# Performance work log

Measured on AMD Instinct MI355X. Metric: run time of the kernel, lower is better.

The kernel has to match this reference:

```python
import jax, jax.numpy as jnp
import numpy as np

NUM_CLASSES = 4
IMG_SIZE = 640.0
NUM_ANCHORS = 3
EPS = 1e-07


def _giou(px, py, pw, ph, tx, ty, tw, th):
    # corners
    x1n, y1n, x1x, y1x = px - pw / 2, py - ph / 2, px + pw / 2, py + ph / 2
    x2n, y2n, x2x, y2x = tx - tw / 2, ty - th / 2, tx + tw / 2, ty + th / 2
    iw = jnp.clip(jnp.minimum(x1x, x2x) - jnp.maximum(x1n, x2n), 0.0)
    ih = jnp.clip(jnp.minimum(y1x, y2x) - jnp.maximum(y1n, y2n), 0.0)
    inter = iw * ih
    union = pw * ph + tw * th - inter + EPS
    iou = inter / union
    ew = jnp.maximum(x1x, x2x) - jnp.minimum(x1n, x2n)
    eh = jnp.maximum(y1x, y2x) - jnp.minimum(y1n, y2n)
    enclose = ew * eh + EPS
    return iou - (enclose - union) / enclose


def _scale_losses(pred, h, w, anc3, targets):
    # pred: [B, 27, h, w]; anc3: [3,2] (pixels); targets: [B,T,5]
    B = pred.shape[0]
    C = pred.shape[1] // NUM_ANCHORS
    p = pred.reshape(B, NUM_ANCHORS, C, h, w).transpose(0, 1, 3, 4, 2)  # [B,A,h,w,C]
    grid_x = (jnp.arange(w, dtype=p.dtype) / w)[None, None, None, :]
    grid_y = (jnp.arange(h, dtype=p.dtype) / h)[None, None, :, None]
    pred_x = jax.nn.sigmoid(p[..., 0]) + grid_x
    pred_y = jax.nn.sigmoid(p[..., 1]) + grid_y
    pred_w = jnp.exp(p[..., 2]) * (anc3[:, 0] / IMG_SIZE).reshape(1, -1, 1, 1)
    pred_h = jnp.exp(p[..., 3]) * (anc3[:, 1] / IMG_SIZE).reshape(1, -1, 1, 1)
    z_conf = p[..., 4]
    z_cls = p[..., 5:5 + NUM_CLASSES]

    cls_id = targets[..., 0].astype(jnp.int32)                      # [B,T]
    tx, ty, tw, th = (targets[..., i] for i in range(1, 5))
    valid = ((tx >= 0) & (tx <= 1) & (ty >= 0) & (ty <= 1) &
             (tw > 0) & (tw <= 1) & (th > 0) & (th <= 1))

    # anchor matching on (w,h) IoU, argmax keeps first max like the loop
    aw = anc3[:, 0] / IMG_SIZE                                      # [A]
    ah = anc3[:, 1] / IMG_SIZE
    inter = jnp.minimum(tw[..., None], aw) * jnp.minimum(th[..., None], ah)
    union = tw[..., None] * th[..., None] + aw * ah - inter
    best = jnp.argmax(inter / (union + EPS), axis=-1)               # [B,T]

    gxi = jnp.clip(jnp.floor(tx * w).astype(jnp.int32), 0, w - 1)
    gyi = jnp.clip(jnp.floor(ty * h).astype(jnp.int32), 0, h - 1)
    b_idx = jnp.arange(B)[:, None]

    px = pred_x[b_idx, best, gyi, gxi]
    py = pred_y[b_idx, best, gyi, gxi]
    pw_ = pred_w[b_idx, best, gyi, gxi]
    ph_ = pred_h[b_idx, best, gyi, gxi]
    zc = z_conf[b_idx, best, gyi, gxi]                              # conf logit [B,T]
    zcl = z_cls[b_idx, best, gyi, gxi]                              # cls logits [B,T,NC]

    giou = _giou(px, py, pw_, ph_, tx, ty, tw, th)
    mask = (valid & (cls_id < NUM_CLASSES)).astype(p.dtype)

    box = jnp.sum(mask * (1.0 - giou))
    onehot = jax.nn.one_hot(cls_id, NUM_CLASSES, dtype=p.dtype)
    # BCE(sigmoid(z), t) = softplus(z) - t*z, mean over classes
    cls_bce = jnp.mean(jax.nn.softplus(zcl) - onehot * zcl, axis=-1)
    cls = jnp.sum(mask * cls_bce)
    conf_t = jnp.clip(jax.lax.stop_gradient(giou), 0.0, 1.0)
    conf = jnp.sum(mask * (jax.nn.softplus(zc) - conf_t * zc))
    n = jnp.sum(valid.astype(p.dtype))
    return box, cls, conf, n


def _neg_conf(pred, h, w, neg_idx):
    # negative-sample conf BCE vs 0: softplus(logit); per-image mean, summed over B
    B = pred.shape[0]
    C = pred.shape[1] // NUM_ANCHORS
    zc = pred.reshape(B, NUM_ANCHORS, C, h, w)[:, :, 4].reshape(B, -1)  # [B, A*h*w]
    taken = jnp.take_along_axis(zc, neg_idx.astype(jnp.int32), axis=1)  # [B,500]
    per_b = jnp.mean(jax.nn.softplus(taken), axis=1)                    # [B]
    n_neg = B * neg_idx.shape[1]
    return 0.5 * jnp.sum(per_b) / n_neg


def yolo_loss(p3_out, p4_out, p5_out, targets, anchors,
              neg_idx_p3, neg_idx_p4, neg_idx_p5):
    scales = [(80, 80, p3_out, 0, neg_idx_p3),
              (40, 40, p4_out, 3, neg_idx_p4),
              (20, 20, p5_out, 6, neg_idx_p5)]
    box = cls = conf = n = jnp.float32(0.0)
    for h, w, pred, a0, _ in scales:
        b, c, cf, nn_ = _scale_losses(pred, h, w, anchors[a0:a0 + 3], targets)
        box, cls, conf, n = box + b, cls + c, conf + cf, n + nn_
    denom = jnp.maximum(n, 1.0)
    has = (n > 0).astype(box.dtype)
    box = jnp.where(n > 0, box / denom, box)
    cls = jnp.where(n > 0, cls / denom, cls)
    conf = jnp.where(n > 0, conf / denom, conf)
    for h, w, pred, a0, nidx in scales:
        conf = conf + _neg_conf(pred, h, w, nidx)
    total = box + cls + conf
    return total, box, cls, conf


def setup_inputs() -> dict:
    key = jax.random.key(0)
    k = jax.random.split(key, 10)
    B, T = 64, 50
    p3 = jax.random.normal(k[0], (B, 27, 80, 80), jnp.float32)
    p4 = jax.random.normal(k[1], (B, 27, 40, 40), jnp.float32)
    p5 = jax.random.normal(k[2], (B, 27, 20, 20), jnp.float32)
    cls = jax.random.randint(k[3], (B, T), 0, NUM_CLASSES).astype(jnp.float32)
    xy = jax.random.uniform(k[4], (B, T, 2), jnp.float32)
    wh = jax.random.uniform(k[5], (B, T, 2), jnp.float32, 0.02, 0.5)
    targets = jnp.concatenate([cls[..., None], xy, wh], axis=-1)
    anchors = jnp.array([[10, 13], [16, 30], [33, 23], [30, 61], [62, 45],
                         [59, 119], [116, 90], [156, 198], [373, 326]], jnp.float32)
    neg3 = jax.random.randint(k[6], (B, 500), 0, 3 * 80 * 80, jnp.int32)
    neg4 = jax.random.randint(k[7], (B, 500), 0, 3 * 40 * 40, jnp.int32)
    neg5 = jax.random.randint(k[8], (B, 500), 0, 3 * 20 * 20, jnp.int32)
    return {"p3_out": p3, "p4_out": p4, "p5_out": p5, "targets": targets,
            "anchors": anchors, "neg_idx_p3": neg3, "neg_idx_p4": neg4,
            "neg_idx_p5": neg5}


def reference(p3_out, p4_out, p5_out, targets, anchors,
              neg_idx_p3, neg_idx_p4, neg_idx_p5):
    return yolo_loss(p3_out, p4_out, p5_out, targets, anchors,
                     neg_idx_p3, neg_idx_p4, neg_idx_p5)
```

## Files before the change

### kernel.cpp

```cpp
#include <hip/hip_runtime.h>
#include <math.h>

#define NUM_CLASSES 4
#define EPS 1e-7f
#define B_ 64
#define T_ 50
#define NNEG 500
#define NPOSB 38
#define NNEGB 94
#define NBLK (NPOSB + NNEGB)
#define MAGIC 0x13579BDFu
#define WSTRIDE 8

__device__ __forceinline__ float softplusf(float x) {
    return fmaxf(x, 0.0f) + log1pf(expf(-fabsf(x)));
}

__global__ void __launch_bounds__(256) yolo_fused(
        const float* __restrict__ pr3, const float* __restrict__ pr4,
        const float* __restrict__ pr5, const float* __restrict__ targets,
        const float* __restrict__ anchors,
        const int* __restrict__ ng3, const int* __restrict__ ng4,
        const int* __restrict__ ng5, float* __restrict__ ws,
        float* __restrict__ out) {
    __shared__ float sred[5][256];

    const int bid = blockIdx.x;
    const int tid = threadIdx.x;

    float v0 = 0.f, v1 = 0.f, v2 = 0.f, v3 = 0.f, v4 = 0.f;

    if (bid < NPOSB) {
        int idx = bid * 256 + tid;
        if (idx < 3 * B_ * T_) {
            int s   = idx / (B_ * T_);
            int rem = idx - s * (B_ * T_);
            int b   = rem / T_;
            int t   = rem - b * T_;

            int hw = (s == 0) ? 80 : ((s == 1) ? 40 : 20);
            const float* pred = (s == 0) ? pr3 : ((s == 1) ? pr4 : pr5);
            int a0 = 3 * s;

            const float* tg = targets + (size_t)(b * T_ + t) * 5;
            float clsf = tg[0], tx = tg[1], ty = tg[2], tw = tg[3], th = tg[4];

            bool valid = (tx >= 0.f) && (tx <= 1.f) && (ty >= 0.f) && (ty <= 1.f) &&
                         (tw > 0.f)  && (tw <= 1.f) && (th > 0.f)  && (th <= 1.f);

            int best = 0; float bestv = -1.f, awb = 0.f, ahb = 0.f;
            #pragma unroll
            for (int a = 0; a < 3; ++a) {
                float aw = anchors[(a0 + a) * 2 + 0] / 640.0f;
                float ah = anchors[(a0 + a) * 2 + 1] / 640.0f;
                float inter = fminf(tw, aw) * fminf(th, ah);
                float uni   = tw * th + aw * ah - inter;
                float r     = inter / (uni + EPS);
                if (r > bestv) { bestv = r; best = a; awb = aw; ahb = ah; }
            }

            int w = hw, h = hw;
            int gxi = (int)floorf(tx * (float)w); gxi = min(max(gxi, 0), w - 1);
            int gyi = (int)floorf(ty * (float)h); gyi = min(max(gyi, 0), h - 1);

            size_t chs = (size_t)h * (size_t)w;
            const float* base = pred + ((size_t)(b * 27 + best * 9) * (size_t)h + (size_t)gyi) * (size_t)w + (size_t)gxi;
            float c0 = base[0 * chs], c1 = base[1 * chs], c2 = base[2 * chs];
            float c3 = base[3 * chs], zc = base[4 * chs];
            float z0 = base[5 * chs], z1 = base[6 * chs];
            float z2 = base[7 * chs], z3 = base[8 * chs];

            float px  = 1.f / (1.f + expf(-c0)) + (float)gxi / (float)w;
            float py  = 1.f / (1.f + expf(-c1)) + (float)gyi / (float)h;
            float pw_ = expf(c2) * awb;
            float ph_ = expf(c3) * ahb;

            float x1n = px - pw_ * 0.5f, x1x = px + pw_ * 0.5f;
            float y1n = py - ph_ * 0.5f, y1x = py + ph_ * 0.5f;
            float x2n = tx - tw * 0.5f,  x2x = tx + tw * 0.5f;
            float y2n = ty - th * 0.5f,  y2x = ty + th * 0.5f;
            float iw = fmaxf(fminf(x1x, x2x) - fmaxf(x1n, x2n), 0.f);
            float ih = fmaxf(fminf(y1x, y2x) - fmaxf(y1n, y2n), 0.f);
            float inter = iw * ih;
            float uni = pw_ * ph_ + tw * th - inter + EPS;
            float iou = inter / uni;
            float ew = fmaxf(x1x, x2x) - fminf(x1n, x2n);
            float eh = fmaxf(y1x, y2x) - fminf(y1n, y2n);
            float enclose = ew * eh + EPS;
            float giou = iou - (enclose - uni) / enclose;

            int cid = (int)clsf;
            float mask = (valid && (cid < NUM_CLASSES)) ? 1.f : 0.f;

            v0 = mask * (1.f - giou);

            float sbce = softplusf(z0) + softplusf(z1) + softplusf(z2) + softplusf(z3);
            float zsel = (cid == 0) ? z0 : (cid == 1) ? z1 : (cid == 2) ? z2 : (cid == 3) ? z3 : 0.f;
            v1 = mask * 0.25f * (sbce - zsel);

            float conf_t = fminf(fmaxf(giou, 0.f), 1.f);
            v2 = mask * (softplusf(zc) - conf_t * zc);

            v3 = valid ? 1.f : 0.f;
        }
    } else {
        int gi = (bid - NPOSB) * 256 + tid;
        if (gi < 24000) {
            int e0  = gi * 4;
            int s   = e0 / (B_ * NNEG);
            int rem = e0 - s * (B_ * NNEG);
            int b   = rem / NNEG;
            int j   = rem - b * NNEG;

            int hw = (s == 0) ? 80 : ((s == 1) ? 40 : 20);
            int chs = hw * hw;
            const float* pred = (s == 0) ? pr3 : ((s == 1) ? pr4 : pr5);
            const int* nix = (s == 0) ? ng3 : ((s == 1) ? ng4 : ng5);

            int4 id4 = *(const int4*)(nix + b * NNEG + j);

            const float* pb = pred + (size_t)(b * 27) * (size_t)chs;
            int ia0 = id4.x / chs, ia1 = id4.y / chs, ia2 = id4.z / chs, ia3 = id4.w / chs;
            float za = pb[(size_t)(ia0 * 9 + 4) * (size_t)chs + (id4.x - ia0 * chs)];
            float zb = pb[(size_t)(ia1 * 9 + 4) * (size_t)chs + (id4.y - ia1 * chs)];
            float zc2 = pb[(size_t)(ia2 * 9 + 4) * (size_t)chs + (id4.z - ia2 * chs)];
            float zd = pb[(size_t)(ia3 * 9 + 4) * (size_t)chs + (id4.w - ia3 * chs)];
            v4 = softplusf(za) + softplusf(zb) + softplusf(zc2) + softplusf(zd);
        }
    }

    sred[0][tid] = v0; sred[1][tid] = v1; sred[2][tid] = v2;
    sred[3][tid] = v3; sred[4][tid] = v4;
    __syncthreads();
    for (int s = 128; s > 0; s >>= 1) {
        if (tid < s) {
            sred[0][tid] += sred[0][tid + s];
            sred[1][tid] += sred[1][tid + s];
            sred[2][tid] += sred[2][tid + s];
            sred[3][tid] += sred[3][tid + s];
            sred[4][tid] += sred[4][tid + s];
        }
        __syncthreads();
    }
    if (tid == 0) {
        float* slot = ws + (size_t)bid * WSTRIDE;
        slot[0] = sred[0][0]; slot[1] = sred[1][0]; slot[2] = sred[2][0];
        slot[3] = sred[3][0]; slot[4] = sred[4][0];
        __hip_atomic_store((unsigned int*)(slot + 5), MAGIC,
                           __ATOMIC_RELEASE, __HIP_MEMORY_SCOPE_AGENT);
    }

    if (bid != 0) return;

    float a0 = 0.f, a1 = 0.f, a2 = 0.f, a3 = 0.f, a4 = 0.f;
    {
        int i = tid;
        if (i < NBLK) {
            unsigned int* flag = (unsigned int*)(ws + (size_t)i * WSTRIDE + 5);
            while (__hip_atomic_load(flag, __ATOMIC_ACQUIRE,
                                     __HIP_MEMORY_SCOPE_AGENT) != MAGIC) {
                __builtin_amdgcn_s_sleep(1);
            }
            const float* slot = ws + (size_t)i * WSTRIDE;
            a0 += slot[0]; a1 += slot[1]; a2 += slot[2];
            a3 += slot[3]; a4 += slot[4];
            *flag = 0u;
        }
    }
    __syncthreads();
    sred[0][tid] = a0; sred[1][tid] = a1; sred[2][tid] = a2;
    sred[3][tid] = a3; sred[4][tid] = a4;
    __syncthreads();
    for (int s = 128; s > 0; s >>= 1) {
        if (tid < s) {
            sred[0][tid] += sred[0][tid + s];
            sred[1][tid] += sred[1][tid + s];
            sred[2][tid] += sred[2][tid + s];
            sred[3][tid] += sred[3][tid + s];
            sred[4][tid] += sred[4][tid + s];
        }
        __syncthreads();
    }
    if (tid == 0) {
        float box = sred[0][0], cls = sred[1][0], conf = sred[2][0];
        float nn = sred[3][0], negsum = sred[4][0];
        float denom = fmaxf(nn, 1.f);
        if (nn > 0.f) { box /= denom; cls /= denom; conf /= denom; }
        float neg = 0.5f * negsum / ((float)NNEG * (float)(B_ * NNEG));
        conf += neg;
        out[0] = box + cls + conf; out[1] = box; out[2] = cls; out[3] = conf;
    }
}

extern "C" void kernel_launch(void* const* d_in, const int* in_sizes, int n_in,
                              void* d_out, int out_size, void* d_ws, size_t ws_size,
                              hipStream_t stream) {
    const float* p3      = (const float*)d_in[0];
    const float* p4      = (const float*)d_in[1];
    const float* p5      = (const float*)d_in[2];
    const float* targets = (const float*)d_in[3];
    const float* anchors = (const float*)d_in[4];
    const int*   ng3     = (const int*)d_in[5];
    const int*   ng4     = (const int*)d_in[6];
    const int*   ng5     = (const int*)d_in[7];

    yolo_fused<<<dim3(NBLK), dim3(256), 0, stream>>>(
        p3, p4, p5, targets, anchors, ng3, ng4, ng5,
        (float*)d_ws, (float*)d_out);
}
```

Before: 12.77 us.

## Split per-target work across thread pairs and use wave-shuffle reductions

Each positive target is now handled by two threads: one computes the box GIoU and objectness terms, the other the class BCE. Each negative thread now gathers two samples instead of four, which roughly doubles the block count. The shared-memory tree reduction is replaced by 64-wide shuffle reductions plus a tiny per-wave shared array. A dedicated extra block does the final cross-block spin-wait reduction instead of block 0. The aim is to cut per-thread gather latency and reduction barriers in this latency-bound kernel. The cost is duplicated index and anchor-matching math, and one more block that spins waiting on the others.

```diff
diff --git a/kernel.cpp b/kernel.cpp
--- a/kernel.cpp
+++ b/kernel.cpp
@@ -6,14 +6,22 @@
 #define B_ 64
 #define T_ 50
 #define NNEG 500
-#define NPOSB 38
-#define NNEGB 94
-#define NBLK (NPOSB + NNEGB)
+#define NPOSB 75
+#define NNEGB 188
+#define NWORK (NPOSB + NNEGB)
+#define NBLK (NWORK + 1)
 #define MAGIC 0x13579BDFu
 #define WSTRIDE 8
 
 __device__ __forceinline__ float softplusf(float x) {
     return fmaxf(x, 0.0f) + log1pf(expf(-fabsf(x)));
+}
+
+__device__ __forceinline__ float wave_reduce(float v) {
+    #pragma unroll
+    for (int off = 32; off > 0; off >>= 1)
+        v += __shfl_down(v, off, 64);
+    return v;
 }
 
 __global__ void __launch_bounds__(256) yolo_fused(
@@ -23,7 +31,7 @@
         const int* __restrict__ ng3, const int* __restrict__ ng4,
         const int* __restrict__ ng5, float* __restrict__ ws,
         float* __restrict__ out) {
-    __shared__ float sred[5][256];
+    __shared__ float sacc[5][4];
 
     const int bid = blockIdx.x;
     const int tid = threadIdx.x;
@@ -31,44 +39,48 @@
     float v0 = 0.f, v1 = 0.f, v2 = 0.f, v3 = 0.f, v4 = 0.f;
 
     if (bid < NPOSB) {
-        int idx = bid * 256 + tid;
-        if (idx < 3 * B_ * T_) {
-            int s   = idx / (B_ * T_);
-            int rem = idx - s * (B_ * T_);
-            int b   = rem / T_;
-            int t   = rem - b * T_;
-
-            int hw = (s == 0) ? 80 : ((s == 1) ? 40 : 20);
-            const float* pred = (s == 0) ? pr3 : ((s == 1) ? pr4 : pr5);
-            int a0 = 3 * s;
-
-            const float* tg = targets + (size_t)(b * T_ + t) * 5;
-            float clsf = tg[0], tx = tg[1], ty = tg[2], tw = tg[3], th = tg[4];
-
-            bool valid = (tx >= 0.f) && (tx <= 1.f) && (ty >= 0.f) && (ty <= 1.f) &&
-                         (tw > 0.f)  && (tw <= 1.f) && (th > 0.f)  && (th <= 1.f);
-
-            int best = 0; float bestv = -1.f, awb = 0.f, ahb = 0.f;
-            #pragma unroll
-            for (int a = 0; a < 3; ++a) {
-                float aw = anchors[(a0 + a) * 2 + 0] / 640.0f;
-                float ah = anchors[(a0 + a) * 2 + 1] / 640.0f;
-                float inter = fminf(tw, aw) * fminf(th, ah);
-                float uni   = tw * th + aw * ah - inter;
-                float r     = inter / (uni + EPS);
-                if (r > bestv) { bestv = r; best = a; awb = aw; ahb = ah; }
-            }
-
-            int w = hw, h = hw;
-            int gxi = (int)floorf(tx * (float)w); gxi = min(max(gxi, 0), w - 1);
-            int gyi = (int)floorf(ty * (float)h); gyi = min(max(gyi, 0), h - 1);
-
-            size_t chs = (size_t)h * (size_t)w;
-            const float* base = pred + ((size_t)(b * 27 + best * 9) * (size_t)h + (size_t)gyi) * (size_t)w + (size_t)gxi;
+        int g = bid * 256 + tid;
+        int p = g >> 1;
+        bool evn = (g & 1) == 0;
+
+        int s   = p / (B_ * T_);
+        int rem = p - s * (B_ * T_);
+        int b   = rem / T_;
+        int t   = rem - b * T_;
+
+        int hw = (s == 0) ? 80 : ((s == 1) ? 40 : 20);
+        const float* pred = (s == 0) ? pr3 : ((s == 1) ? pr4 : pr5);
+        int a0 = 3 * s;
+
+        const float* tg = targets + (size_t)(b * T_ + t) * 5;
+        float clsf = tg[0], tx = tg[1], ty = tg[2], tw = tg[3], th = tg[4];
+
+        bool valid = (tx >= 0.f) && (tx <= 1.f) && (ty >= 0.f) && (ty <= 1.f) &&
+                     (tw > 0.f)  && (tw <= 1.f) && (th > 0.f)  && (th <= 1.f);
+        int cid = (int)clsf;
+        float mask = (valid && (cid < NUM_CLASSES)) ? 1.f : 0.f;
+
+        int best = 0; float bestv = -1.f, awb = 0.f, ahb = 0.f;
+        #pragma unroll
+        for (int a = 0; a < 3; ++a) {
+            float aw = anchors[(a0 + a) * 2 + 0] / 640.0f;
+            float ah = anchors[(a0 + a) * 2 + 1] / 640.0f;
+            float inter = fminf(tw, aw) * fminf(th, ah);
+            float uni   = tw * th + aw * ah - inter;
+            float r     = inter / (uni + EPS);
+            if (r > bestv) { bestv = r; best = a; awb = aw; ahb = ah; }
+        }
+
+        int w = hw, h = hw;
+        int gxi = (int)floorf(tx * (float)w); gxi = min(max(gxi, 0), w - 1);
+        int gyi = (int)floorf(ty * (float)h); gyi = min(max(gyi, 0), h - 1);
+
+        size_t chs = (size_t)h * (size_t)w;
+        const float* base = pred + ((size_t)(b * 27 + best * 9) * (size_t)h + (size_t)gyi) * (size_t)w + (size_t)gxi;
+
+        if (evn) {
             float c0 = base[0 * chs], c1 = base[1 * chs], c2 = base[2 * chs];
             float c3 = base[3 * chs], zc = base[4 * chs];
-            float z0 = base[5 * chs], z1 = base[6 * chs];
-            float z2 = base[7 * chs], z3 = base[8 * chs];
 
             float px  = 1.f / (1.f + expf(-c0)) + (float)gxi / (float)w;
             float py  = 1.f / (1.f + expf(-c1)) + (float)gyi / (float)h;
@@ -89,24 +101,21 @@
             float enclose = ew * eh + EPS;
             float giou = iou - (enclose - uni) / enclose;
 
-            int cid = (int)clsf;
-            float mask = (valid && (cid < NUM_CLASSES)) ? 1.f : 0.f;
-
             v0 = mask * (1.f - giou);
-
+            float conf_t = fminf(fmaxf(giou, 0.f), 1.f);
+            v2 = mask * (softplusf(zc) - conf_t * zc);
+            v3 = valid ? 1.f : 0.f;
+        } else {
+            float z0 = base[5 * chs], z1 = base[6 * chs];
+            float z2 = base[7 * chs], z3 = base[8 * chs];
             float sbce = softplusf(z0) + softplusf(z1) + softplusf(z2) + softplusf(z3);
             float zsel = (cid == 0) ? z0 : (cid == 1) ? z1 : (cid == 2) ? z2 : (cid == 3) ? z3 : 0.f;
             v1 = mask * 0.25f * (sbce - zsel);
-
-            float conf_t = fminf(fmaxf(giou, 0.f), 1.f);
-            v2 = mask * (softplusf(zc) - conf_t * zc);
-
-            v3 = valid ? 1.f : 0.f;
-        }
-    } else {
+        }
+    } else if (bid < NWORK) {
         int gi = (bid - NPOSB) * 256 + tid;
-        if (gi < 24000) {
-            int e0  = gi * 4;
+        if (gi < 48000) {
+            int e0  = gi * 2;
             int s   = e0 / (B_ * NNEG);
             int rem = e0 - s * (B_ * NNEG);
             int b   = rem / NNEG;
@@ -117,45 +126,17 @@
             const float* pred = (s == 0) ? pr3 : ((s == 1) ? pr4 : pr5);
             const int* nix = (s == 0) ? ng3 : ((s == 1) ? ng4 : ng5);
 
-            int4 id4 = *(const int4*)(nix + b * NNEG + j);
+            int2 id2 = *(const int2*)(nix + b * NNEG + j);
 
             const float* pb = pred + (size_t)(b * 27) * (size_t)chs;
-            int ia0 = id4.x / chs, ia1 = id4.y / chs, ia2 = id4.z / chs, ia3 = id4.w / chs;
-            float za = pb[(size_t)(ia0 * 9 + 4) * (size_t)chs + (id4.x - ia0 * chs)];
-            float zb = pb[(size_t)(ia1 * 9 + 4) * (size_t)chs + (id4.y - ia1 * chs)];
-            float zc2 = pb[(size_t)(ia2 * 9 + 4) * (size_t)chs + (id4.z - ia2 * chs)];
-            float zd = pb[(size_t)(ia3 * 9 + 4) * (size_t)chs + (id4.w - ia3 * chs)];
-            v4 = softplusf(za) + softplusf(zb) + softplusf(zc2) + softplusf(zd);
-        }
-    }
-
-    sred[0][tid] = v0; sred[1][tid] = v1; sred[2][tid] = v2;
-    sred[3][tid] = v3; sred[4][tid] = v4;
-    __syncthreads();
-    for (int s = 128; s > 0; s >>= 1) {
-        if (tid < s) {
-            sred[0][tid] += sred[0][tid + s];
-            sred[1][tid] += sred[1][tid + s];
-            sred[2][tid] += sred[2][tid + s];
-            sred[3][tid] += sred[3][tid + s];
-            sred[4][tid] += sred[4][tid + s];
-        }
-        __syncthreads();
-    }
-    if (tid == 0) {
-        float* slot = ws + (size_t)bid * WSTRIDE;
-        slot[0] = sred[0][0]; slot[1] = sred[1][0]; slot[2] = sred[2][0];
-        slot[3] = sred[3][0]; slot[4] = sred[4][0];
-        __hip_atomic_store((unsigned int*)(slot + 5), MAGIC,
-                           __ATOMIC_RELEASE, __HIP_MEMORY_SCOPE_AGENT);
-    }
-
-    if (bid != 0) return;
-
-    float a0 = 0.f, a1 = 0.f, a2 = 0.f, a3 = 0.f, a4 = 0.f;
-    {
-        int i = tid;
-        if (i < NBLK) {
+            int ia0 = id2.x / chs, ia1 = id2.y / chs;
+            float za = pb[(size_t)(ia0 * 9 + 4) * (size_t)chs + (id2.x - ia0 * chs)];
+            float zb = pb[(size_t)(ia1 * 9 + 4) * (size_t)chs + (id2.y - ia1 * chs)];
+            v4 = softplusf(za) + softplusf(zb);
+        }
+    } else {
+        float a0 = 0.f, a1 = 0.f, a2 = 0.f, a3 = 0.f, a4 = 0.f;
+        for (int i = tid; i < NWORK; i += 256) {
             unsigned int* flag = (unsigned int*)(ws + (size_t)i * WSTRIDE + 5);
             while (__hip_atomic_load(flag, __ATOMIC_ACQUIRE,
                                      __HIP_MEMORY_SCOPE_AGENT) != MAGIC) {
@@ -166,29 +147,45 @@
             a3 += slot[3]; a4 += slot[4];
             *flag = 0u;
         }
+        a0 = wave_reduce(a0); a1 = wave_reduce(a1); a2 = wave_reduce(a2);
+        a3 = wave_reduce(a3); a4 = wave_reduce(a4);
+        int lane = tid & 63, wid = tid >> 6;
+        if (lane == 0) {
+            sacc[0][wid] = a0; sacc[1][wid] = a1; sacc[2][wid] = a2;
+            sacc[3][wid] = a3; sacc[4][wid] = a4;
+        }
+        __syncthreads();
+        if (tid == 0) {
+            float box = sacc[0][0] + sacc[0][1] + sacc[0][2] + sacc[0][3];
+            float cls = sacc[1][0] + sacc[1][1] + sacc[1][2] + sacc[1][3];
+            float cnf = sacc[2][0] + sacc[2][1] + sacc[2][2] + sacc[2][3];
+            float nn  = sacc[3][0] + sacc[3][1] + sacc[3][2] + sacc[3][3];
+            float ng  = sacc[4][0] + sacc[4][1] + sacc[4][2] + sacc[4][3];
+            float denom = fmaxf(nn, 1.f);
+            if (nn > 0.f) { box /= denom; cls /= denom; cnf /= denom; }
+            cnf += 0.5f * ng / ((float)NNEG * (float)(B_ * NNEG));
+            out[0] = box + cls + cnf; out[1] = box; out[2] = cls; out[3] = cnf;
+        }
+        return;
+    }
+
+    v0 = wave_reduce(v0); v1 = wave_reduce(v1); v2 = wave_reduce(v2);
+    v3 = wave_reduce(v3); v4 = wave_reduce(v4);
+    int lane = tid & 63, wid = tid >> 6;
+    if (lane == 0) {
+        sacc[0][wid] = v0; sacc[1][wid] = v1; sacc[2][wid] = v2;
+        sacc[3][wid] = v3; sacc[4][wid] = v4;
     }
     __syncthreads();
-    sred[0][tid] = a0; sred[1][tid] = a1; sred[2][tid] = a2;
-    sred[3][tid] = a3; sred[4][tid] = a4;
-    __syncthreads();
-    for (int s = 128; s > 0; s >>= 1) {
-        if (tid < s) {
-            sred[0][tid] += sred[0][tid + s];
-            sred[1][tid] += sred[1][tid + s];
-            sred[2][tid] += sred[2][tid + s];
-            sred[3][tid] += sred[3][tid + s];
-            sred[4][tid] += sred[4][tid + s];
-        }
-        __syncthreads();
-    }
     if (tid == 0) {
-        float box = sred[0][0], cls = sred[1][0], conf = sred[2][0];
-        float nn = sred[3][0], negsum = sred[4][0];
-        float denom = fmaxf(nn, 1.f);
-        if (nn > 0.f) { box /= denom; cls /= denom; conf /= denom; }
-        float neg = 0.5f * negsum / ((float)NNEG * (float)(B_ * NNEG));
-        conf += neg;
-        out[0] = box + cls + conf; out[1] = box; out[2] = cls; out[3] = conf;
+        float* slot = ws + (size_t)bid * WSTRIDE;
+        slot[0] = sacc[0][0] + sacc[0][1] + sacc[0][2] + sacc[0][3];
+        slot[1] = sacc[1][0] + sacc[1][1] + sacc[1][2] + sacc[1][3];
+        slot[2] = sacc[2][0] + sacc[2][1] + sacc[2][2] + sacc[2][3];
+        slot[3] = sacc[3][0] + sacc[3][1] + sacc[3][2] + sacc[3][3];
+        slot[4] = sacc[4][0] + sacc[4][1] + sacc[4][2] + sacc[4][3];
+        __hip_atomic_store((unsigned int*)(slot + 5), MAGIC,
+                           __ATOMIC_RELEASE, __HIP_MEMORY_SCOPE_AGENT);
     }
 }
 
```

After: 17.80 us. 39.4% more time.
